# Optimization experiments

Hardware: AMD Instinct MI355X
Metric: run time of the kernel (lower is better)

The kernel has to match this reference:

```python
import jax, jax.numpy as jnp
import numpy as np
from jax.scipy.special import logsumexp

T, NT = 16384, 1024


def setup_inputs() -> dict:
    key = jax.random.key(0)
    k1, k2, k3, k4, k5 = jax.random.split(key, 5)
    return {
        "emit": jax.random.normal(k1, (T, NT), dtype=jnp.float32),
        "y": jax.random.randint(k2, (T,), 0, NT),
        "trans": jax.random.normal(k3, (NT, NT), dtype=jnp.float32),
        "strans": jax.random.normal(k4, (NT,), dtype=jnp.float32),
        "etrans": jax.random.normal(k5, (NT,), dtype=jnp.float32),
    }


def reference(emit, y, trans, strans, etrans):
    # Forward (log-partition) via logsumexp scan over time.
    # torch step: scores = (trans + emit[i]).T; alpha = logsumexp(scores + alpha, dim=1)
    # i.e. alpha_new[k] = emit[i, k] + logsumexp_j(alpha[j] + trans[j, k])
    def step(alpha, e_t):
        alpha_new = e_t + logsumexp(alpha[:, None] + trans, axis=0)
        return alpha_new, None

    alpha0 = strans + emit[0]
    alpha, _ = jax.lax.scan(step, alpha0, emit[1:])
    logZ = logsumexp(alpha + etrans)

    # Gold-path score
    t = emit.shape[0]
    score = (
        strans[y[0]]
        + trans[y[:-1], y[1:]].sum()
        + etrans[y[-1]]
        + emit[jnp.arange(t), y].sum()
    )
    return logZ - score
```

## Files before the change

### kernel.cpp

```cpp
#include <hip/hip_runtime.h>

#define T_LEN 16384
#define NT 1024
#define NBLK 64
#define CPB 16
#define NTHR 256
#define MID 8191

typedef unsigned long long u64;
typedef unsigned int u32;
typedef __attribute__((ext_vector_type(4))) u32 u32x4;

__device__ __align__(32) u64 g_fbuf[2 * NT];
__device__ __align__(32) u64 g_bbuf[2 * NT];

__device__ __forceinline__ u64 pack_tag(u32 tag, float v) {
  return ((u64)tag << 32) | (u64)__float_as_uint(v);
}
__device__ __forceinline__ u64 ld_tag(const u64* p) {
  return __hip_atomic_load(p, __ATOMIC_RELAXED, __HIP_MEMORY_SCOPE_AGENT);
}
__device__ __forceinline__ void st_tag(u64* p, u64 v) {
  __hip_atomic_store(p, v, __ATOMIC_RELAXED, __HIP_MEMORY_SCOPE_AGENT);
}

__device__ __forceinline__ void ld8_dev(const u64* q, u32x4& A, u32x4& B) {
  asm volatile("global_load_dwordx4 %0, %2, off sc0 sc1\n\t"
               "global_load_dwordx4 %1, %2, off offset:16 sc0 sc1\n\t"
               "s_waitcnt vmcnt(0)"
               : "=&v"(A), "=&v"(B)
               : "v"(q)
               : "memory");
}

__global__ __launch_bounds__(1024) void crf_init(const float* __restrict__ emit,
                                                 const float* __restrict__ strans,
                                                 const float* __restrict__ etrans) {
  int tid = threadIdx.x;
  g_fbuf[tid] = pack_tag(0u, strans[tid] + emit[tid]);
  g_bbuf[tid] = pack_tag(0u, etrans[tid] + emit[(T_LEN - 1) * NT + tid]);
}

__global__ __launch_bounds__(1024) void crf_score(const float* __restrict__ emit,
                                                  const int* __restrict__ y,
                                                  const float* __restrict__ trans,
                                                  const float* __restrict__ strans,
                                                  const float* __restrict__ etrans,
                                                  float* __restrict__ ws) {
  int tid = threadIdx.x;
  float local = 0.f;
  for (int t = tid; t < T_LEN; t += 1024) {
    int yt = y[t];
    local += emit[t * NT + yt];
    if (t > 0) local += trans[y[t - 1] * NT + yt];
  }
  if (tid == 0) local += strans[y[0]];
  if (tid == 1023) local += etrans[y[T_LEN - 1]];
#pragma unroll
  for (int o = 32; o; o >>= 1) local += __shfl_xor(local, o);
  __shared__ float sm[16];
  if ((tid & 63) == 0) sm[tid >> 6] = local;
  __syncthreads();
  if (tid == 0) {
    float s = 0.f;
    for (int i = 0; i < 16; ++i) s += sm[i];
    ws[4096] = s;
  }
}

__global__ __launch_bounds__(NTHR, 1) void crf_scan(const float* __restrict__ emit,
                                                    const float* __restrict__ trans) {
  const int tid = threadIdx.x;
  const bool fwd = blockIdx.x < NBLK;
  const int blk = fwd ? blockIdx.x : (blockIdx.x - NBLK);

  const int c = tid & 15;
  const int chunk = tid >> 4;
  const int col = blk * CPB + c;
  const int wv = tid >> 6;

  u64* buf0 = fwd ? g_fbuf : g_bbuf;
  u64* buf1 = buf0 + NT;
  const int STEPS = fwd ? MID : (T_LEN - 1 - MID);

  float p[64];
  const int jbase = chunk * 64;
#pragma unroll
  for (int i = 0; i < 16; ++i) {
    int off = (4 * i + 8 * chunk) & 63;
#pragma unroll
    for (int x = 0; x < 4; ++x) {
      int jj = jbase + off + x;
      float tv = fwd ? trans[jj * NT + col] : trans[col * NT + jj];
      p[4 * i + x] = __expf(tv);
    }
  }

  __shared__ __align__(16) float aS[NT];
  __shared__ float partS[64];

  float M;
  {
    u64 wd = ld_tag(buf0 + col);
    float v = __uint_as_float((u32)wd);
#pragma unroll
    for (int o = 8; o; o >>= 1) v = fmaxf(v, __shfl_xor(v, o));
    M = v;
  }

  for (int n = 1; n <= STEPS; ++n) {
    u64* bIn  = (n & 1) ? buf0 : buf1;
    u64* bOut = (n & 1) ? buf1 : buf0;

    const int te = fwd ? n : (T_LEN - 1 - n);
    float e = emit[te * NT + col];

    const u32 want = (u32)(n - 1);
    const u64* q = bIn + (tid << 2);
    u32x4 A, B;
    for (;;) {
      ld8_dev(q, A, B);
      if (!((A.y ^ want) | (A.w ^ want) | (B.y ^ want) | (B.w ^ want))) break;
    }
    float4 av;
    av.x = __expf(__uint_as_float(A.x) - M);
    av.y = __expf(__uint_as_float(A.z) - M);
    av.z = __expf(__uint_as_float(B.x) - M);
    av.w = __expf(__uint_as_float(B.z) - M);
    ((float4*)aS)[tid] = av;
    __syncthreads();

    float s = 0.f;
    const float4* aV = (const float4*)aS;
#pragma unroll
    for (int i = 0; i < 16; ++i) {
      int off = (4 * i + 8 * chunk) & 63;
      float4 a4 = aV[(jbase + off) >> 2];
      s = fmaf(a4.x, p[4 * i + 0], s);
      s = fmaf(a4.y, p[4 * i + 1], s);
      s = fmaf(a4.z, p[4 * i + 2], s);
      s = fmaf(a4.w, p[4 * i + 3], s);
    }
    s += __shfl_xor(s, 16);
    s += __shfl_xor(s, 32);
    if ((tid & 63) < 16) partS[wv * 16 + c] = s;
    __syncthreads();

    float tot = partS[c] + partS[16 + c] + partS[32 + c] + partS[48 + c];
    float anew = e + M + __logf(tot);
    if (tid < 16) st_tag(bOut + col, pack_tag((u32)n, anew));

    float m2 = anew;
#pragma unroll
    for (int o = 8; o; o >>= 1) m2 = fmaxf(m2, __shfl_xor(m2, o));
    M = m2;
  }
}

__global__ __launch_bounds__(1024) void crf_final(const float* __restrict__ emit,
                                                  const float* __restrict__ ws,
                                                  float* __restrict__ out) {
  int tid = threadIdx.x;
  float fa = __uint_as_float((u32)g_fbuf[NT + tid]);
  float bb = __uint_as_float((u32)g_bbuf[tid]);
  float v = fa + bb - emit[MID * NT + tid];
  float m = v;
#pragma unroll
  for (int o = 32; o; o >>= 1) m = fmaxf(m, __shfl_xor(m, o));
  __shared__ float sm[16];
  __shared__ float sM;
  if ((tid & 63) == 0) sm[tid >> 6] = m;
  __syncthreads();
  if (tid == 0) {
    float mm = sm[0];
    for (int i = 1; i < 16; ++i) mm = fmaxf(mm, sm[i]);
    sM = mm;
  }
  __syncthreads();
  float Mv = sM;
  float s = __expf(v - Mv);
#pragma unroll
  for (int o = 32; o; o >>= 1) s += __shfl_xor(s, o);
  __shared__ float ss[16];
  if ((tid & 63) == 0) ss[tid >> 6] = s;
  __syncthreads();
  if (tid == 0) {
    float tot = 0.f;
    for (int i = 0; i < 16; ++i) tot += ss[i];
    float logZ = Mv + __logf(tot);
    out[0] = logZ - ws[4096];
  }
}

extern "C" void kernel_launch(void* const* d_in, const int* in_sizes, int n_in,
                              void* d_out, int out_size, void* d_ws, size_t ws_size,
                              hipStream_t stream) {
  const float* emit = (const float*)d_in[0];
  const int* y = (const int*)d_in[1];
  const float* trans = (const float*)d_in[2];
  const float* strans = (const float*)d_in[3];
  const float* etrans = (const float*)d_in[4];
  float* ws = (float*)d_ws;
  float* out = (float*)d_out;

  crf_init<<<1, 1024, 0, stream>>>(emit, strans, etrans);
  crf_score<<<1, 1024, 0, stream>>>(emit, y, trans, strans, etrans, ws);
  crf_scan<<<2 * NBLK, NTHR, 0, stream>>>(emit, trans);
  crf_final<<<1, 1024, 0, stream>>>(emit, ws, out);
}
```

Measured before the change: 12.66 ms.

## Pipeline tag polling loads, drop block barrier, split FMA accumulators

Measured after the change: 13.38 ms. +5.7%, slower.

```diff
diff --git a/kernel.cpp b/kernel.cpp
--- a/kernel.cpp
+++ b/kernel.cpp
@@ -24,13 +24,20 @@
   __hip_atomic_store(p, v, __ATOMIC_RELAXED, __HIP_MEMORY_SCOPE_AGENT);
 }
 
-__device__ __forceinline__ void ld8_dev(const u64* q, u32x4& A, u32x4& B) {
+__device__ __forceinline__ void ld8_issue(const u64* q, u32x4& A, u32x4& B) {
   asm volatile("global_load_dwordx4 %0, %2, off sc0 sc1\n\t"
-               "global_load_dwordx4 %1, %2, off offset:16 sc0 sc1\n\t"
-               "s_waitcnt vmcnt(0)"
+               "global_load_dwordx4 %1, %2, off offset:16 sc0 sc1"
                : "=&v"(A), "=&v"(B)
                : "v"(q)
                : "memory");
+}
+__device__ __forceinline__ void vm_wait2(u32x4& A, u32x4& B) {
+  asm volatile("s_waitcnt vmcnt(2)" : "+v"(A), "+v"(B));
+  __builtin_amdgcn_sched_barrier(0);
+}
+__device__ __forceinline__ void vm_wait0() {
+  asm volatile("s_waitcnt vmcnt(0)" ::: "memory");
+  __builtin_amdgcn_sched_barrier(0);
 }
 
 __global__ __launch_bounds__(1024) void crf_init(const float* __restrict__ emit,
@@ -117,30 +124,52 @@
 
     const u32 want = (u32)(n - 1);
     const u64* q = bIn + (tid << 2);
-    u32x4 A, B;
+    u32x4 A0, B0, A1, B1;
+    ld8_issue(q, A0, B0);
+    ld8_issue(q, A1, B1);
+    float4 av;
     for (;;) {
-      ld8_dev(q, A, B);
-      if (!((A.y ^ want) | (A.w ^ want) | (B.y ^ want) | (B.w ^ want))) break;
+      vm_wait2(A0, B0);
+      if (!((A0.y ^ want) | (A0.w ^ want) | (B0.y ^ want) | (B0.w ^ want))) {
+        av.x = __uint_as_float(A0.x); av.y = __uint_as_float(A0.z);
+        av.z = __uint_as_float(B0.x); av.w = __uint_as_float(B0.z);
+        break;
+      }
+      ld8_issue(q, A0, B0);
+      vm_wait2(A1, B1);
+      if (!((A1.y ^ want) | (A1.w ^ want) | (B1.y ^ want) | (B1.w ^ want))) {
+        av.x = __uint_as_float(A1.x); av.y = __uint_as_float(A1.z);
+        av.z = __uint_as_float(B1.x); av.w = __uint_as_float(B1.z);
+        break;
+      }
+      ld8_issue(q, A1, B1);
     }
-    float4 av;
-    av.x = __expf(__uint_as_float(A.x) - M);
-    av.y = __expf(__uint_as_float(A.z) - M);
-    av.z = __expf(__uint_as_float(B.x) - M);
-    av.w = __expf(__uint_as_float(B.z) - M);
+    vm_wait0();
+    av.x = __expf(av.x - M);
+    av.y = __expf(av.y - M);
+    av.z = __expf(av.z - M);
+    av.w = __expf(av.w - M);
     ((float4*)aS)[tid] = av;
-    __syncthreads();
-
-    float s = 0.f;
+
+
+    float s0 = 0.f, s1 = 0.f;
     const float4* aV = (const float4*)aS;
 #pragma unroll
-    for (int i = 0; i < 16; ++i) {
-      int off = (4 * i + 8 * chunk) & 63;
-      float4 a4 = aV[(jbase + off) >> 2];
-      s = fmaf(a4.x, p[4 * i + 0], s);
-      s = fmaf(a4.y, p[4 * i + 1], s);
-      s = fmaf(a4.z, p[4 * i + 2], s);
-      s = fmaf(a4.w, p[4 * i + 3], s);
+    for (int i = 0; i < 16; i += 2) {
+      int offA = (4 * i + 8 * chunk) & 63;
+      int offB = (4 * i + 4 + 8 * chunk) & 63;
+      float4 a4 = aV[(jbase + offA) >> 2];
+      float4 b4 = aV[(jbase + offB) >> 2];
+      s0 = fmaf(a4.x, p[4 * i + 0], s0);
+      s0 = fmaf(a4.y, p[4 * i + 1], s0);
+      s0 = fmaf(a4.z, p[4 * i + 2], s0);
+      s0 = fmaf(a4.w, p[4 * i + 3], s0);
+      s1 = fmaf(b4.x, p[4 * i + 4], s1);
+      s1 = fmaf(b4.y, p[4 * i + 5], s1);
+      s1 = fmaf(b4.z, p[4 * i + 6], s1);
+      s1 = fmaf(b4.w, p[4 * i + 7], s1);
     }
+    float s = s0 + s1;
     s += __shfl_xor(s, 16);
     s += __shfl_xor(s, 32);
     if ((tid & 63) < 16) partS[wv * 16 + c] = s;
```

## Drop redundant block barrier and prefetch next poll load in CRF scan

Applied to the files above, without the earlier changes.

New measurement: 15.54 ms. 1.23x slower.

```diff
diff --git a/kernel.cpp b/kernel.cpp
--- a/kernel.cpp
+++ b/kernel.cpp
@@ -24,13 +24,16 @@
   __hip_atomic_store(p, v, __ATOMIC_RELAXED, __HIP_MEMORY_SCOPE_AGENT);
 }
 
-__device__ __forceinline__ void ld8_dev(const u64* q, u32x4& A, u32x4& B) {
+__device__ __forceinline__ void ld8_issue(const u64* q, u32x4& A, u32x4& B) {
   asm volatile("global_load_dwordx4 %0, %2, off sc0 sc1\n\t"
-               "global_load_dwordx4 %1, %2, off offset:16 sc0 sc1\n\t"
-               "s_waitcnt vmcnt(0)"
+               "global_load_dwordx4 %1, %2, off offset:16 sc0 sc1"
                : "=&v"(A), "=&v"(B)
                : "v"(q)
                : "memory");
+}
+__device__ __forceinline__ void vm_wait0p(u32x4& A, u32x4& B) {
+  asm volatile("s_waitcnt vmcnt(0)" : "+v"(A), "+v"(B) :: "memory");
+  __builtin_amdgcn_sched_barrier(0);
 }
 
 __global__ __launch_bounds__(1024) void crf_init(const float* __restrict__ emit,
@@ -108,6 +111,9 @@
     M = v;
   }
 
+  u32x4 A, B;
+  ld8_issue(buf0 + (tid << 2), A, B);
+
   for (int n = 1; n <= STEPS; ++n) {
     u64* bIn  = (n & 1) ? buf0 : buf1;
     u64* bOut = (n & 1) ? buf1 : buf0;
@@ -117,10 +123,10 @@
 
     const u32 want = (u32)(n - 1);
     const u64* q = bIn + (tid << 2);
-    u32x4 A, B;
     for (;;) {
-      ld8_dev(q, A, B);
+      vm_wait0p(A, B);
       if (!((A.y ^ want) | (A.w ^ want) | (B.y ^ want) | (B.w ^ want))) break;
+      ld8_issue(q, A, B);
     }
     float4 av;
     av.x = __expf(__uint_as_float(A.x) - M);
@@ -128,19 +134,26 @@
     av.z = __expf(__uint_as_float(B.x) - M);
     av.w = __expf(__uint_as_float(B.z) - M);
     ((float4*)aS)[tid] = av;
-    __syncthreads();
-
-    float s = 0.f;
+
+
+    float s0 = 0.f, s1 = 0.f;
     const float4* aV = (const float4*)aS;
 #pragma unroll
-    for (int i = 0; i < 16; ++i) {
-      int off = (4 * i + 8 * chunk) & 63;
-      float4 a4 = aV[(jbase + off) >> 2];
-      s = fmaf(a4.x, p[4 * i + 0], s);
-      s = fmaf(a4.y, p[4 * i + 1], s);
-      s = fmaf(a4.z, p[4 * i + 2], s);
-      s = fmaf(a4.w, p[4 * i + 3], s);
+    for (int i = 0; i < 16; i += 2) {
+      int offA = (4 * i + 8 * chunk) & 63;
+      int offB = (4 * i + 4 + 8 * chunk) & 63;
+      float4 a4 = aV[(jbase + offA) >> 2];
+      float4 b4 = aV[(jbase + offB) >> 2];
+      s0 = fmaf(a4.x, p[4 * i + 0], s0);
+      s0 = fmaf(a4.y, p[4 * i + 1], s0);
+      s0 = fmaf(a4.z, p[4 * i + 2], s0);
+      s0 = fmaf(a4.w, p[4 * i + 3], s0);
+      s1 = fmaf(b4.x, p[4 * i + 4], s1);
+      s1 = fmaf(b4.y, p[4 * i + 5], s1);
+      s1 = fmaf(b4.z, p[4 * i + 6], s1);
+      s1 = fmaf(b4.w, p[4 * i + 7], s1);
     }
+    float s = s0 + s1;
     s += __shfl_xor(s, 16);
     s += __shfl_xor(s, 32);
     if ((tid & 63) < 16) partS[wv * 16 + c] = s;
@@ -149,6 +162,8 @@
     float tot = partS[c] + partS[16 + c] + partS[32 + c] + partS[48 + c];
     float anew = e + M + __logf(tot);
     if (tid < 16) st_tag(bOut + col, pack_tag((u32)n, anew));
+
+    ld8_issue(bOut + (tid << 2), A, B);
 
     float m2 = anew;
 #pragma unroll
```
